# Kernel optimization log

Hardware: AMD Instinct MI355X
Metric: run time of the kernel (lower is better)

## Reference

```python
import jax, jax.numpy as jnp
import numpy as np
import math

N, C, H, W = 4, 256, 64, 64
CH = C // 2  # theta/phi output channels


def setup_inputs() -> dict:
    key = jax.random.key(0)
    k1, k2, k3 = jax.random.split(key, 3)
    x = jax.random.normal(k1, (N, C, H, W), dtype=jnp.float32)
    # 1x1 conv weights, init normal(0, 0.01) as in reset_params
    theta_w = 0.01 * jax.random.normal(k2, (CH, C), dtype=jnp.float32)
    phi_w = 0.01 * jax.random.normal(k3, (CH, C), dtype=jnp.float32)
    theta_b = jnp.zeros((CH,), dtype=jnp.float32)
    phi_b = jnp.zeros((CH,), dtype=jnp.float32)
    return {"x": x, "theta_w": theta_w, "theta_b": theta_b, "phi_w": phi_w, "phi_b": phi_b}


def reference(x, theta_w, theta_b, phi_w, phi_b):
    n, c, h, w = x.shape
    hw = h * w
    scale = 1.0 / math.sqrt(c)  # divide by sqrt(self.in_ch)
    # 1x1 convs (pointwise channel mixes)
    q = jnp.einsum('nchw,dc->ndhw', x, theta_w) + theta_b[None, :, None, None]
    k = jnp.einsum('nchw,dc->ndhw', x, phi_w) + phi_b[None, :, None, None]
    # affinity: [n, hw, hw] (flattened 'nabcd' tensor)
    q2 = q.reshape(n, c // 2, hw)
    k2 = k.reshape(n, c // 2, hw)
    ff = jnp.einsum('nis,nit->nst', q2, k2) * scale
    attn = jax.nn.softmax(ff, axis=-1)
    # weighted sum of values x: out[n,i,s] = sum_t attn[n,s,t] x[n,i,t]
    out = jnp.einsum('nst,nit->nis', attn, x.reshape(n, c, hw))
    return out.reshape(x.shape)
```

## Files before the change

kernel.cpp:

```cpp
#include <hip/hip_runtime.h>

#define S_LEN 4096
#define C_CH  256
#define D_CH  128
#define LAMBDA 0.09016844005555896f

typedef __attribute__((ext_vector_type(8)))  short short8;
typedef __attribute__((ext_vector_type(4)))  float f32x4;
typedef __attribute__((ext_vector_type(16))) float f32x16;

union PFrag { unsigned u[4]; short8 v; };

static __device__ __forceinline__ unsigned short f2bf(float x) {
    union { float f; unsigned u; } v; v.f = x;
    unsigned r = v.u + 0x7FFFu + ((v.u >> 16) & 1u);
    return (unsigned short)(r >> 16);
}
static __device__ __forceinline__ float bf2f(unsigned short b) {
    union { unsigned u; float f; } v; v.u = ((unsigned)b) << 16; return v.f;
}

static __device__ __forceinline__ void gload_lds16(const void* g, void* l) {
    __builtin_amdgcn_global_load_lds(
        (const __attribute__((address_space(1))) void*)g,
        (__attribute__((address_space(3))) void*)l, 16, 0, 0);
}

__global__ void nlm_wconv_kernel(const float* __restrict__ tw, const float* __restrict__ pw,
                                 unsigned short* __restrict__ wb) {
    int base = (blockIdx.x * 256 + threadIdx.x) * 4;
    const float* src = (base < 32768) ? (tw + base) : (pw + base - 32768);
    float4 v = *reinterpret_cast<const float4*>(src);
    ushort4 b; b.x = f2bf(v.x); b.y = f2bf(v.y); b.z = f2bf(v.z); b.w = f2bf(v.w);
    *reinterpret_cast<ushort4*>(wb + base) = b;
}

__launch_bounds__(256, 1)
__global__ void nlm_proj_kernel(const float* __restrict__ x,
                                const unsigned short* __restrict__ wb,
                                const float* __restrict__ tb, const float* __restrict__ pbias,
                                unsigned char* __restrict__ Qb8, unsigned char* __restrict__ Kb8,
                                unsigned short* __restrict__ xb) {
    const int n    = blockIdx.y;
    const int wave = threadIdx.x >> 6;
    const int lane = threadIdx.x & 63;
    const int sl   = lane & 15, g = lane >> 4;
    const int s0   = blockIdx.x * 64 + wave * 16;
    const float* xn = x + (size_t)n * C_CH * S_LEN;
    unsigned short* xbn = xb + (size_t)n * C_CH * S_LEN;

    f32x4 acc[16];
    #pragma unroll
    for (int i = 0; i < 16; ++i) acc[i] = (f32x4){0.f, 0.f, 0.f, 0.f};

    #pragma unroll 1
    for (int cc = 0; cc < 8; ++cc) {
        short8 af;
        #pragma unroll
        for (int j = 0; j < 8; ++j) {
            float v = xn[(size_t)(cc * 32 + g * 8 + j) * S_LEN + s0 + sl];
            af[j] = (short)f2bf(v);
        }
        #pragma unroll
        for (int j = 0; j < 8; ++j) {
            xbn[(size_t)(cc * 32 + g * 8 + j) * S_LEN + s0 + sl] = (unsigned short)af[j];
        }
        #pragma unroll
        for (int t = 0; t < 16; ++t) {
            const unsigned short* wp = wb + (size_t)(t >> 3) * (D_CH * C_CH)
                                          + (size_t)((t & 7) * 16 + sl) * C_CH + cc * 32 + g * 8;
            short8 bf = *reinterpret_cast<const short8*>(wp);
            acc[t] = __builtin_amdgcn_mfma_f32_16x16x32_bf16(af, bf, acc[t], 0, 0, 0);
        }
    }
    #pragma unroll
    for (int t = 0; t < 16; ++t) {
        const float bias = (t < 8 ? tb : pbias)[(t & 7) * 16 + sl];
        unsigned char* dst = (t < 8 ? Qb8 : Kb8) + (size_t)n * S_LEN * D_CH;
        const int col = (t & 7) * 16 + sl;
        float v0 = acc[t][0] + bias, v1 = acc[t][1] + bias;
        float v2 = acc[t][2] + bias, v3 = acc[t][3] + bias;
        unsigned u01, u23;
        asm("v_cvt_pk_fp8_f32 %0, %1, %2" : "=v"(u01) : "v"(v0), "v"(v1));
        asm("v_cvt_pk_fp8_f32 %0, %1, %2" : "=v"(u23) : "v"(v2), "v"(v3));
        dst[(size_t)(s0 + g * 4 + 0) * D_CH + col] = (unsigned char)(u01 & 0xff);
        dst[(size_t)(s0 + g * 4 + 1) * D_CH + col] = (unsigned char)((u01 >> 8) & 0xff);
        dst[(size_t)(s0 + g * 4 + 2) * D_CH + col] = (unsigned char)(u23 & 0xff);
        dst[(size_t)(s0 + g * 4 + 3) * D_CH + col] = (unsigned char)((u23 >> 8) & 0xff);
    }
}

template<int TSPLIT>
__launch_bounds__(512, 2)
__global__ void nlm_attn_kernel(const unsigned char* __restrict__ Qb8,
                                const unsigned char* __restrict__ Kb8,
                                const unsigned short* __restrict__ xb,
                                unsigned short* __restrict__ part0,
                                unsigned short* __restrict__ part1,
                                unsigned short* __restrict__ part2,
                                unsigned short* __restrict__ part3,
                                float* __restrict__ lbuf) {
    constexpr int TRANGE = S_LEN / TSPLIT;
    constexpr int NITv   = TRANGE / 64;
    constexpr int TOTAL  = 64 * TSPLIT;
    const int sid  = blockIdx.x;
    const int newb = (sid & 7) * (TOTAL / 8) + (sid >> 3);
    const int n    = newb / (16 * TSPLIT);
    const int th   = (newb >> 4) & (TSPLIT - 1);
    const int sb   = newb & 15;
    const int lane = threadIdx.x & 63;
    const int wave = threadIdx.x >> 6;
    const int l31  = lane & 31;
    const int h    = lane >> 5;
    const int s0   = sb * 256 + wave * 32;
    const int tbase = th * TRANGE;

    __shared__ unsigned char  Klds[2][64 * 128];
    __shared__ unsigned short Vlds[2][256 * 64];

    const unsigned char* Qn8 = Qb8 + (size_t)n * S_LEN * D_CH;
    const unsigned char* Kn8 = Kb8 + (size_t)n * S_LEN * D_CH;
    const unsigned short* xn = xb + (size_t)n * C_CH * S_LEN;

    long qf8[8];
    #pragma unroll
    for (int ks = 0; ks < 8; ++ks)
        qf8[ks] = *reinterpret_cast<const long*>(Qn8 + (size_t)(s0 + l31) * D_CH + ks * 16 + h * 8);

    f32x16 oacc[8];
    #pragma unroll
    for (int i = 0; i < 8; ++i)
        #pragma unroll
        for (int r = 0; r < 16; ++r) oacc[i][r] = 0.f;
    float lsum = 0.f;

    auto kstage = [&](int itv, int slot) {
        const int it = itv < NITv ? itv : NITv - 1;
        const int t0 = tbase + it * 64;
        const int rl = wave * 8 + (lane >> 3);
        const int ch = (lane & 7) ^ ((rl ^ (rl >> 3)) & 7);
        gload_lds16(Kn8 + (size_t)(t0 + rl) * D_CH + ch * 16,
                    &Klds[slot][wave * 8 * 128]);
    };
    auto vstage = [&](int itv, int slot) {
        const int it = itv < NITv ? itv : NITv - 1;
        const int t0 = tbase + it * 64;
        #pragma unroll
        for (int i = 0; i < 4; ++i) {
            const int row = wave * 32 + i * 8 + (lane >> 3);
            const int ch = (lane & 7) ^ ((row ^ (row >> 3)) & 7);
            gload_lds16(xn + (size_t)row * S_LEN + t0 + ch * 8,
                        &Vlds[slot][(wave * 32 + i * 8) * 64]);
        }
    };

    kstage(0, 0); vstage(0, 0);
    asm volatile("s_waitcnt vmcnt(0)" ::: "memory");

    const int flo = (l31 ^ (l31 >> 3)) & 7;
    const int fhi = flo ^ 4;

    #pragma unroll 1
    for (int it = 0; it < NITv; ++it) {
        const int cur = it & 1;
        __builtin_amdgcn_s_barrier();
        __builtin_amdgcn_sched_barrier(0);
        kstage(it + 1, cur ^ 1);
        vstage(it + 1, cur ^ 1);

        f32x16 sa, sb2;
        #pragma unroll
        for (int r = 0; r < 16; ++r) { sa[r] = 0.f; sb2[r] = 0.f; }
        __builtin_amdgcn_s_setprio(1);
        #pragma unroll
        for (int ks = 0; ks < 8; ++ks) {
            const int clo = ((ks ^ flo) * 16) + h * 8;
            const int chi = ((ks ^ fhi) * 16) + h * 8;
            long kflo = *reinterpret_cast<const long*>(&Klds[cur][l31 * 128 + clo]);
            long kfhi = *reinterpret_cast<const long*>(&Klds[cur][(32 + l31) * 128 + chi]);
            sa  = __builtin_amdgcn_mfma_f32_32x32x16_fp8_fp8(kflo, qf8[ks], sa,  0, 0, 0);
            sb2 = __builtin_amdgcn_mfma_f32_32x32x16_fp8_fp8(kfhi, qf8[ks], sb2, 0, 0, 0);
        }
        __builtin_amdgcn_s_setprio(0);

        PFrag pa0, pa1, pa2, pa3;
        float rs = 0.f;
        {
            float p[16];
            #pragma unroll
            for (int r = 0; r < 16; ++r) { p[r] = __builtin_amdgcn_exp2f(sa[r] * LAMBDA); rs += p[r]; }
            unsigned W0, W1, W2, W3, W4, W5, W6, W7;
            asm("v_cvt_pk_bf16_f32 %0, %1, %2" : "=v"(W0) : "v"(p[0]),  "v"(p[1]));
            asm("v_cvt_pk_bf16_f32 %0, %1, %2" : "=v"(W1) : "v"(p[2]),  "v"(p[3]));
            asm("v_cvt_pk_bf16_f32 %0, %1, %2" : "=v"(W2) : "v"(p[4]),  "v"(p[5]));
            asm("v_cvt_pk_bf16_f32 %0, %1, %2" : "=v"(W3) : "v"(p[6]),  "v"(p[7]));
            asm("v_cvt_pk_bf16_f32 %0, %1, %2" : "=v"(W4) : "v"(p[8]),  "v"(p[9]));
            asm("v_cvt_pk_bf16_f32 %0, %1, %2" : "=v"(W5) : "v"(p[10]), "v"(p[11]));
            asm("v_cvt_pk_bf16_f32 %0, %1, %2" : "=v"(W6) : "v"(p[12]), "v"(p[13]));
            asm("v_cvt_pk_bf16_f32 %0, %1, %2" : "=v"(W7) : "v"(p[14]), "v"(p[15]));
            asm("v_permlane32_swap_b32 %0, %1" : "+v"(W0), "+v"(W2));
            asm("v_permlane32_swap_b32 %0, %1" : "+v"(W1), "+v"(W3));
            asm("v_permlane32_swap_b32 %0, %1" : "+v"(W4), "+v"(W6));
            asm("v_permlane32_swap_b32 %0, %1" : "+v"(W5), "+v"(W7));
            pa0.u[0] = W0; pa0.u[1] = W1; pa0.u[2] = W2; pa0.u[3] = W3;
            pa1.u[0] = W4; pa1.u[1] = W5; pa1.u[2] = W6; pa1.u[3] = W7;
        }

        __builtin_amdgcn_s_setprio(1);
        #pragma unroll
        for (int cb = 0; cb < 8; ++cb) {
            const int c = cb * 32 + l31;
            const unsigned short* Vr = &Vlds[cur][c * 64];
            const int fv = flo ^ ((cb & 1) << 2);
            short8 vf0 = *reinterpret_cast<const short8*>(&Vr[((0 + h) ^ fv) * 8]);
            short8 vf1 = *reinterpret_cast<const short8*>(&Vr[((2 + h) ^ fv) * 8]);
            oacc[cb] = __builtin_amdgcn_mfma_f32_32x32x16_bf16(vf0, pa0.v, oacc[cb], 0, 0, 0);
            oacc[cb] = __builtin_amdgcn_mfma_f32_32x32x16_bf16(vf1, pa1.v, oacc[cb], 0, 0, 0);
        }
        __builtin_amdgcn_s_setprio(0);

        {
            float p[16];
            #pragma unroll
            for (int r = 0; r < 16; ++r) { p[r] = __builtin_amdgcn_exp2f(sb2[r] * LAMBDA); rs += p[r]; }
            unsigned W0, W1, W2, W3, W4, W5, W6, W7;
            asm("v_cvt_pk_bf16_f32 %0, %1, %2" : "=v"(W0) : "v"(p[0]),  "v"(p[1]));
            asm("v_cvt_pk_bf16_f32 %0, %1, %2" : "=v"(W1) : "v"(p[2]),  "v"(p[3]));
            asm("v_cvt_pk_bf16_f32 %0, %1, %2" : "=v"(W2) : "v"(p[4]),  "v"(p[5]));
            asm("v_cvt_pk_bf16_f32 %0, %1, %2" : "=v"(W3) : "v"(p[6]),  "v"(p[7]));
            asm("v_cvt_pk_bf16_f32 %0, %1, %2" : "=v"(W4) : "v"(p[8]),  "v"(p[9]));
            asm("v_cvt_pk_bf16_f32 %0, %1, %2" : "=v"(W5) : "v"(p[10]), "v"(p[11]));
            asm("v_cvt_pk_bf16_f32 %0, %1, %2" : "=v"(W6) : "v"(p[12]), "v"(p[13]));
            asm("v_cvt_pk_bf16_f32 %0, %1, %2" : "=v"(W7) : "v"(p[14]), "v"(p[15]));
            asm("v_permlane32_swap_b32 %0, %1" : "+v"(W0), "+v"(W2));
            asm("v_permlane32_swap_b32 %0, %1" : "+v"(W1), "+v"(W3));
            asm("v_permlane32_swap_b32 %0, %1" : "+v"(W4), "+v"(W6));
            asm("v_permlane32_swap_b32 %0, %1" : "+v"(W5), "+v"(W7));
            pa2.u[0] = W0; pa2.u[1] = W1; pa2.u[2] = W2; pa2.u[3] = W3;
            pa3.u[0] = W4; pa3.u[1] = W5; pa3.u[2] = W6; pa3.u[3] = W7;
        }
        lsum += rs;

        __builtin_amdgcn_s_setprio(1);
        #pragma unroll
        for (int cb = 0; cb < 8; ++cb) {
            const int c = cb * 32 + l31;
            const unsigned short* Vr = &Vlds[cur][c * 64];
            const int fv = flo ^ ((cb & 1) << 2);
            short8 vf2 = *reinterpret_cast<const short8*>(&Vr[((4 + h) ^ fv) * 8]);
            short8 vf3 = *reinterpret_cast<const short8*>(&Vr[((6 + h) ^ fv) * 8]);
            oacc[cb] = __builtin_amdgcn_mfma_f32_32x32x16_bf16(vf2, pa2.v, oacc[cb], 0, 0, 0);
            oacc[cb] = __builtin_amdgcn_mfma_f32_32x32x16_bf16(vf3, pa3.v, oacc[cb], 0, 0, 0);
        }
        __builtin_amdgcn_s_setprio(0);

        asm volatile("s_waitcnt vmcnt(0)" ::: "memory");
        __builtin_amdgcn_sched_barrier(0);
    }

    float lt = lsum + __shfl_xor(lsum, 32);
    unsigned short* dst = (th == 0) ? part0 : (th == 1) ? part1 : (th == 2) ? part2 : part3;
    if (lane < 32) lbuf[th * 16384 + n * 4096 + s0 + lane] = lt;
    unsigned short* on = dst + (size_t)n * C_CH * S_LEN;
    #pragma unroll
    for (int cb = 0; cb < 8; ++cb) {
        #pragma unroll
        for (int r = 0; r < 16; ++r) {
            const int c = cb * 32 + (r & 3) + 8 * (r >> 2) + 4 * h;
            on[(size_t)c * S_LEN + s0 + l31] = f2bf(oacc[cb][r]);
        }
    }
}

template<int TSPLIT>
__global__ void nlm_combine_kernel(float* __restrict__ out,
                                   const unsigned short* __restrict__ p0,
                                   const unsigned short* __restrict__ p1,
                                   const unsigned short* __restrict__ p2,
                                   const unsigned short* __restrict__ p3,
                                   const float* __restrict__ lbuf) {
    const size_t e0 = ((size_t)blockIdx.x * 256 + threadIdx.x) * 4;
    const int n = (int)(e0 >> 20);
    const int s = (int)(e0 & 4095);
    ushort4 a = *reinterpret_cast<const ushort4*>(p0 + e0);
    ushort4 b = *reinterpret_cast<const ushort4*>(p1 + e0);
    float4 l0 = *reinterpret_cast<const float4*>(lbuf + n * 4096 + s);
    float4 l1 = *reinterpret_cast<const float4*>(lbuf + 16384 + n * 4096 + s);
    float4 o, l;
    o.x = bf2f(a.x) + bf2f(b.x); o.y = bf2f(a.y) + bf2f(b.y);
    o.z = bf2f(a.z) + bf2f(b.z); o.w = bf2f(a.w) + bf2f(b.w);
    l.x = l0.x + l1.x; l.y = l0.y + l1.y; l.z = l0.z + l1.z; l.w = l0.w + l1.w;
    if (TSPLIT == 4) {
        ushort4 c = *reinterpret_cast<const ushort4*>(p2 + e0);
        ushort4 d = *reinterpret_cast<const ushort4*>(p3 + e0);
        float4 l2 = *reinterpret_cast<const float4*>(lbuf + 2 * 16384 + n * 4096 + s);
        float4 l3 = *reinterpret_cast<const float4*>(lbuf + 3 * 16384 + n * 4096 + s);
        o.x += bf2f(c.x) + bf2f(d.x); o.y += bf2f(c.y) + bf2f(d.y);
        o.z += bf2f(c.z) + bf2f(d.z); o.w += bf2f(c.w) + bf2f(d.w);
        l.x += l2.x + l3.x; l.y += l2.y + l3.y; l.z += l2.z + l3.z; l.w += l2.w + l3.w;
    }
    float4 r;
    r.x = o.x / l.x; r.y = o.y / l.y; r.z = o.z / l.z; r.w = o.w / l.w;
    *reinterpret_cast<float4*>(out + e0) = r;
}

extern "C" void kernel_launch(void* const* d_in, const int* in_sizes, int n_in,
                              void* d_out, int out_size, void* d_ws, size_t ws_size,
                              hipStream_t stream) {
    const float* x  = (const float*)d_in[0];
    const float* tw = (const float*)d_in[1];
    const float* tb = (const float*)d_in[2];
    const float* pw = (const float*)d_in[3];
    const float* pb = (const float*)d_in[4];
    float* out = (float*)d_out;

    char* ws = (char*)d_ws;
    unsigned short* xb  = (unsigned short*)(ws);
    unsigned char*  Qb8 = (unsigned char*)(ws + 8388608);
    unsigned char*  Kb8 = (unsigned char*)(ws + 12582912);
    unsigned short* wb  = (unsigned short*)(ws + 16777216);
    float*          lb  = (float*)(ws + 16908288);
    unsigned short* p0  = (unsigned short*)(ws + 17825792);
    unsigned short* p1  = (unsigned short*)(ws + 26214400);
    unsigned short* p2  = (unsigned short*)(ws + 34603008);
    unsigned short* p3  = (unsigned short*)(ws + 42991616);

    nlm_wconv_kernel<<<64, 256, 0, stream>>>(tw, pw, wb);
    nlm_proj_kernel<<<dim3(64, 4), 256, 0, stream>>>(x, wb, tb, pb, Qb8, Kb8, xb);
    if (ws_size >= (size_t)51380224) {
        nlm_attn_kernel<4><<<256, 512, 0, stream>>>(Qb8, Kb8, xb, p0, p1, p2, p3, lb);
        nlm_combine_kernel<4><<<4096, 256, 0, stream>>>(out, p0, p1, p2, p3, lb);
    } else {
        nlm_attn_kernel<2><<<128, 512, 0, stream>>>(Qb8, Kb8, xb, p0, p1, p0, p0, lb);
        nlm_combine_kernel<2><<<4096, 256, 0, stream>>>(out, p0, p1, p0, p0, lb);
    }
}
```

Before: 88.26 us.

## Fuse split-T combine into attention kernel via cooperative grid sync

Removes the separate combine kernel. Each attention block writes bf16 partials only for the channel blocks it does not own, waits at a cooperative grid-wide barrier, then adds the other splits' partials to its own fp32 accumulators for its owned channel slice and normalizes into the output. This saves one kernel launch and a round trip of its own partial through memory. In exchange it adds a grid sync with fences and requires all 256 blocks to be co-resident under cooperative launch.

```diff
diff --git a/kernel.cpp b/kernel.cpp
--- a/kernel.cpp
+++ b/kernel.cpp
@@ -1,4 +1,5 @@
 #include <hip/hip_runtime.h>
+#include <hip/hip_cooperative_groups.h>
 
 #define S_LEN 4096
 #define C_CH  256
@@ -95,6 +96,7 @@
 __global__ void nlm_attn_kernel(const unsigned char* __restrict__ Qb8,
                                 const unsigned char* __restrict__ Kb8,
                                 const unsigned short* __restrict__ xb,
+                                float* __restrict__ out,
                                 unsigned short* __restrict__ part0,
                                 unsigned short* __restrict__ part1,
                                 unsigned short* __restrict__ part2,
@@ -103,6 +105,7 @@
     constexpr int TRANGE = S_LEN / TSPLIT;
     constexpr int NITv   = TRANGE / 64;
     constexpr int TOTAL  = 64 * TSPLIT;
+    constexpr int QCB    = 8 / TSPLIT;
     const int sid  = blockIdx.x;
     const int newb = (sid & 7) * (TOTAL / 8) + (sid >> 3);
     const int n    = newb / (16 * TSPLIT);
@@ -259,49 +262,44 @@
     }
 
     float lt = lsum + __shfl_xor(lsum, 32);
-    unsigned short* dst = (th == 0) ? part0 : (th == 1) ? part1 : (th == 2) ? part2 : part3;
+    unsigned short* pp_w[4] = {part0, part1, part2, part3};
+    unsigned short* dst = pp_w[th];
     if (lane < 32) lbuf[th * 16384 + n * 4096 + s0 + lane] = lt;
     unsigned short* on = dst + (size_t)n * C_CH * S_LEN;
     #pragma unroll
     for (int cb = 0; cb < 8; ++cb) {
+        if (cb / QCB == th) continue;
         #pragma unroll
         for (int r = 0; r < 16; ++r) {
             const int c = cb * 32 + (r & 3) + 8 * (r >> 2) + 4 * h;
             on[(size_t)c * S_LEN + s0 + l31] = f2bf(oacc[cb][r]);
         }
     }
-}
-
-template<int TSPLIT>
-__global__ void nlm_combine_kernel(float* __restrict__ out,
-                                   const unsigned short* __restrict__ p0,
-                                   const unsigned short* __restrict__ p1,
-                                   const unsigned short* __restrict__ p2,
-                                   const unsigned short* __restrict__ p3,
-                                   const float* __restrict__ lbuf) {
-    const size_t e0 = ((size_t)blockIdx.x * 256 + threadIdx.x) * 4;
-    const int n = (int)(e0 >> 20);
-    const int s = (int)(e0 & 4095);
-    ushort4 a = *reinterpret_cast<const ushort4*>(p0 + e0);
-    ushort4 b = *reinterpret_cast<const ushort4*>(p1 + e0);
-    float4 l0 = *reinterpret_cast<const float4*>(lbuf + n * 4096 + s);
-    float4 l1 = *reinterpret_cast<const float4*>(lbuf + 16384 + n * 4096 + s);
-    float4 o, l;
-    o.x = bf2f(a.x) + bf2f(b.x); o.y = bf2f(a.y) + bf2f(b.y);
-    o.z = bf2f(a.z) + bf2f(b.z); o.w = bf2f(a.w) + bf2f(b.w);
-    l.x = l0.x + l1.x; l.y = l0.y + l1.y; l.z = l0.z + l1.z; l.w = l0.w + l1.w;
-    if (TSPLIT == 4) {
-        ushort4 c = *reinterpret_cast<const ushort4*>(p2 + e0);
-        ushort4 d = *reinterpret_cast<const ushort4*>(p3 + e0);
-        float4 l2 = *reinterpret_cast<const float4*>(lbuf + 2 * 16384 + n * 4096 + s);
-        float4 l3 = *reinterpret_cast<const float4*>(lbuf + 3 * 16384 + n * 4096 + s);
-        o.x += bf2f(c.x) + bf2f(d.x); o.y += bf2f(c.y) + bf2f(d.y);
-        o.z += bf2f(c.z) + bf2f(d.z); o.w += bf2f(c.w) + bf2f(d.w);
-        l.x += l2.x + l3.x; l.y += l2.y + l3.y; l.z += l2.z + l3.z; l.w += l2.w + l3.w;
-    }
-    float4 r;
-    r.x = o.x / l.x; r.y = o.y / l.y; r.z = o.z / l.z; r.w = o.w / l.w;
-    *reinterpret_cast<float4*>(out + e0) = r;
+
+    __threadfence();
+    cooperative_groups::this_grid().sync();
+    __threadfence();
+
+    const unsigned short* pp[4] = {part0, part1, part2, part3};
+    float ltot = 0.f;
+    #pragma unroll
+    for (int t2 = 0; t2 < TSPLIT; ++t2) ltot += lbuf[t2 * 16384 + n * 4096 + s0 + l31];
+    const float li = 1.0f / ltot;
+    #pragma unroll
+    for (int cb = 0; cb < 8; ++cb) {
+        if (cb / QCB != th) continue;
+        #pragma unroll
+        for (int r = 0; r < 16; ++r) {
+            const int c = cb * 32 + (r & 3) + 8 * (r >> 2) + 4 * h;
+            const size_t idx = (size_t)n * C_CH * S_LEN + (size_t)c * S_LEN + s0 + l31;
+            float v = oacc[cb][r];
+            #pragma unroll
+            for (int t2 = 0; t2 < TSPLIT; ++t2) {
+                if (t2 != th) v += bf2f(pp[t2][idx]);
+            }
+            out[idx] = v * li;
+        }
+    }
 }
 
 extern "C" void kernel_launch(void* const* d_in, const int* in_sizes, int n_in,
@@ -328,10 +326,14 @@
     nlm_wconv_kernel<<<64, 256, 0, stream>>>(tw, pw, wb);
     nlm_proj_kernel<<<dim3(64, 4), 256, 0, stream>>>(x, wb, tb, pb, Qb8, Kb8, xb);
     if (ws_size >= (size_t)51380224) {
-        nlm_attn_kernel<4><<<256, 512, 0, stream>>>(Qb8, Kb8, xb, p0, p1, p2, p3, lb);
-        nlm_combine_kernel<4><<<4096, 256, 0, stream>>>(out, p0, p1, p2, p3, lb);
+        void* args[] = {(void*)&Qb8, (void*)&Kb8, (void*)&xb, (void*)&out,
+                        (void*)&p0, (void*)&p1, (void*)&p2, (void*)&p3, (void*)&lb};
+        hipLaunchCooperativeKernel((void*)nlm_attn_kernel<4>, dim3(256), dim3(512),
+                                   args, 0, stream);
     } else {
-        nlm_attn_kernel<2><<<128, 512, 0, stream>>>(Qb8, Kb8, xb, p0, p1, p0, p0, lb);
-        nlm_combine_kernel<2><<<4096, 256, 0, stream>>>(out, p0, p1, p0, p0, lb);
-    }
-}
+        void* args[] = {(void*)&Qb8, (void*)&Kb8, (void*)&xb, (void*)&out,
+                        (void*)&p0, (void*)&p1, (void*)&p1, (void*)&p1, (void*)&lb};
+        hipLaunchCooperativeKernel((void*)nlm_attn_kernel<2>, dim3(128), dim3(512),
+                                   args, 0, stream);
+    }
+}
```

New measurement: 209.4 us. 137% more time.
